# Optimization experiments

Measured on AMD Instinct MI355X. Metric: run time of the kernel, lower is better.

Reference implementation:

```python
import jax, jax.numpy as jnp
import numpy as np

BATCH, NODES, CH_IN, CH_OUT, N_EXPERTS = 8, 8192, 128, 128, 64

def setup_inputs() -> dict:
    key = jax.random.key(0)
    kx, kw, ks = jax.random.split(key, 3)
    x = jax.random.normal(kx, (BATCH, NODES, CH_IN), dtype=jnp.float32)
    # std = fan_in**-0.5 per self_init
    W = jax.random.normal(kw, (N_EXPERTS, CH_OUT, CH_IN), dtype=jnp.float32) * (CH_IN ** -0.5)
    sel = jax.random.randint(ks, (NODES,), 0, N_EXPERTS, dtype=jnp.int64)
    return {"x": x, "sel": sel, "W": W}

def reference(x, sel, W):
    # x: (b, n, j), W[sel]: (n, i, j) -> out: (b, n, i)
    Wsel = W[sel]  # gather a (ch_out, ch_in) matrix per node
    return jnp.einsum('bnj,nij->bni', x, Wsel)
```

## Files before the change

kernel.cpp:

```cpp
#include <hip/hip_runtime.h>

#define BATCH   8
#define NODES   8192
#define CH      128
#define NEXP    64
#define TN      16
#define MAXP    (NODES + NEXP * TN)
#define NTILES  (MAXP / TN)
#define NSORT   64
#define SLICE   (NODES / NSORT)

typedef __attribute__((ext_vector_type(8))) short bf16x8;
typedef __attribute__((ext_vector_type(4))) float f32x4;

typedef const __attribute__((address_space(1))) unsigned int gu32;
typedef __attribute__((address_space(3))) unsigned int lu32;

__device__ __forceinline__ bf16x8 cvt8(f32x4 lo, f32x4 hi) {
    bf16x8 r;
    #pragma unroll
    for (int i = 0; i < 4; ++i) {
        r[i]     = (short)__builtin_bit_cast(unsigned short, static_cast<__bf16>(lo[i]));
        r[i + 4] = (short)__builtin_bit_cast(unsigned short, static_cast<__bf16>(hi[i]));
    }
    return r;
}

__global__ __launch_bounds__(256)
void prep1_kernel(const int* __restrict__ sel, const float* __restrict__ W,
                  short* __restrict__ Wbf, int* __restrict__ sorted,
                  int* __restrict__ gcnt)
{
    const int t   = threadIdx.x;
    const int blk = blockIdx.x;

    #pragma unroll
    for (int i = 0; i < 2; ++i) {
        const int g8  = blk * 512 + i * 256 + t;
        const int e   = g8 >> 11;
        const int row = (g8 & 2047) >> 4;
        const int chk = g8 & 15;
        const float* ws = W + (size_t)g8 * 8;
        f32x4 lo = *reinterpret_cast<const f32x4*>(ws);
        f32x4 hi = *reinterpret_cast<const f32x4*>(ws + 4);
        short* wd = Wbf + ((size_t)e << 14) + row * CH + ((chk ^ (row & 7)) << 3);
        *reinterpret_cast<bf16x8*>(wd) = cvt8(lo, hi);
    }

    {
        const int si = blk * 256 + t;
        if (si < MAXP) sorted[si] = -1;
    }

    if (blk < NSORT) {
        __shared__ int hist[NEXP];
        if (t < NEXP) hist[t] = 0;
        __syncthreads();
        if (t < SLICE) atomicAdd(&hist[sel[blk * SLICE + t]], 1);
        __syncthreads();
        if (t < NEXP) gcnt[blk * NEXP + t] = hist[t];
    }
}

__global__ __launch_bounds__(256)
void prep2_kernel(const int* __restrict__ sel, const int* __restrict__ gcnt,
                  int* __restrict__ sorted)
{
    const int t   = threadIdx.x;
    const int blk = blockIdx.x;

    __shared__ int cursor[NEXP];

    if (t < NEXP) {
        int cnt = 0, own = 0;
        for (int s = 0; s < NSORT; ++s) {
            int g = gcnt[s * NEXP + t];
            own += (s < blk) ? g : 0;
            cnt += g;
        }
        int p = (cnt + TN - 1) & ~(TN - 1);
        int scan = p;
        #pragma unroll
        for (int d = 1; d < NEXP; d <<= 1) {
            int v = __shfl_up(scan, d);
            if (t >= d) scan += v;
        }
        cursor[t] = (scan - p) + own;
    }
    __syncthreads();

    if (t < SLICE) {
        int n = blk * SLICE + t;
        int e = sel[n];
        int pos = atomicAdd(&cursor[e], 1);
        sorted[pos] = n;
    }
}

__global__ __launch_bounds__(256)
void gemm_kernel(const float* __restrict__ x, const int* __restrict__ sel,
                 const short* __restrict__ Wbf, float* __restrict__ out,
                 const int* __restrict__ sorted)
{
    __shared__ short s_w[CH * CH];
    __shared__ int s_nodes[TN];
    __shared__ int s_expert;

    const int tid  = threadIdx.x;
    const int tile = blockIdx.x;

    if (tid < TN) s_nodes[tid] = sorted[tile * TN + tid];
    if (tid == 0) {
        int n0 = sorted[tile * TN];
        s_expert = (n0 >= 0) ? sel[n0] : -1;
    }
    __syncthreads();

    const int e = s_expert;
    if (e < 0) return;

    const int wave = tid >> 6;
    const int lane = tid & 63;
    const int m16  = lane & 15;
    const int quad = lane >> 4;

    int          nodej[2];
    const float* xrow[2];
    #pragma unroll
    for (int jt = 0; jt < 2; ++jt) {
        int j    = wave * 32 + jt * 16 + m16;
        int node = s_nodes[j >> 3];
        int b    = j & 7;
        nodej[jt] = node;
        int nd   = (node >= 0) ? node : 0;
        xrow[jt] = x + ((size_t)(b * NODES + nd)) * CH;
    }

    f32x4 xl[2][4][2];
    #pragma unroll
    for (int jt = 0; jt < 2; ++jt)
        #pragma unroll
        for (int kk = 0; kk < 4; ++kk) {
            const float* p = xrow[jt] + kk * 32 + quad * 8;
            xl[jt][kk][0] = *reinterpret_cast<const f32x4*>(p);
            xl[jt][kk][1] = *reinterpret_cast<const f32x4*>(p + 4);
        }

    {
        const char* gsrc = (const char*)(Wbf + ((size_t)e << 14))
                         + wave * 8192 + lane * 16;
        char* ldst = (char*)s_w + wave * 8192;
        #pragma unroll
        for (int i = 0; i < 8; ++i) {
            __builtin_amdgcn_global_load_lds(
                (gu32*)(gsrc + i * 1024),
                (lu32*)(ldst + i * 1024),
                16, 0, 0);
        }
    }
    __syncthreads();

    bf16x8 xfrag[2][4];
    #pragma unroll
    for (int jt = 0; jt < 2; ++jt)
        #pragma unroll
        for (int kk = 0; kk < 4; ++kk)
            xfrag[jt][kk] = cvt8(xl[jt][kk][0], xl[jt][kk][1]);

    f32x4 acc[2][8];
    #pragma unroll
    for (int jt = 0; jt < 2; ++jt)
        #pragma unroll
        for (int ct = 0; ct < 8; ++ct)
            acc[jt][ct] = (f32x4){0.f, 0.f, 0.f, 0.f};

    #pragma unroll
    for (int kk = 0; kk < 4; ++kk) {
        #pragma unroll
        for (int ct = 0; ct < 8; ++ct) {
            const int row = ct * 16 + m16;
            const bf16x8 wfrag = *reinterpret_cast<const bf16x8*>(
                s_w + row * CH + (((kk * 4 + quad) ^ (row & 7)) << 3));
            acc[0][ct] = __builtin_amdgcn_mfma_f32_16x16x32_bf16(
                             wfrag, xfrag[0][kk], acc[0][ct], 0, 0, 0);
            acc[1][ct] = __builtin_amdgcn_mfma_f32_16x16x32_bf16(
                             wfrag, xfrag[1][kk], acc[1][ct], 0, 0, 0);
        }
    }

    #pragma unroll
    for (int jt = 0; jt < 2; ++jt) {
        int node = nodej[jt];
        if (node < 0) continue;
        int j = wave * 32 + jt * 16 + m16;
        int b = j & 7;
        float* orow = out + ((size_t)(b * NODES + node)) * CH;
        #pragma unroll
        for (int ct = 0; ct < 8; ++ct)
            *reinterpret_cast<f32x4*>(orow + ct * 16 + quad * 4) = acc[jt][ct];
    }
}

extern "C" void kernel_launch(void* const* d_in, const int* in_sizes, int n_in,
                              void* d_out, int out_size, void* d_ws, size_t ws_size,
                              hipStream_t stream)
{
    const float* x   = (const float*)d_in[0];
    const int*   sel = (const int*)  d_in[1];
    const float* W   = (const float*)d_in[2];
    float*       out = (float*)d_out;

    short* Wbf    = (short*)d_ws;
    int*   sorted = (int*)((char*)d_ws + (size_t)NEXP * CH * CH * sizeof(short));
    int*   gcnt   = sorted + MAXP;

    prep1_kernel<<<256, 256, 0, stream>>>(sel, W, Wbf, sorted, gcnt);
    prep2_kernel<<<NSORT, 256, 0, stream>>>(sel, gcnt, sorted);
    gemm_kernel<<<NTILES, 256, 0, stream>>>(x, sel, Wbf, out, sorted);
}
```

Before: 102.2 us.

## Precompute per-tile expert id and drop dependent-load prologue in gemm kernel

The sort pass now writes each tile's expert id into a small array, so the GEMM block reads its expert directly instead of going through sorted→sel. This removes one barrier and a chain of dependent global loads at kernel start. The W tile's async LDS loads are also issued before the x loads, and x loads and output stores use nontemporal hints. prep2 runs with 128 threads and fully unrolls its count loop. The tile-expert array adds a small workspace write during prep.

New measurement: 108.7 us. 1.06x slower.

```diff
diff --git a/kernel.cpp b/kernel.cpp
--- a/kernel.cpp
+++ b/kernel.cpp
@@ -29,7 +29,7 @@
 __global__ __launch_bounds__(256)
 void prep1_kernel(const int* __restrict__ sel, const float* __restrict__ W,
                   short* __restrict__ Wbf, int* __restrict__ sorted,
-                  int* __restrict__ gcnt)
+                  int* __restrict__ texp, int* __restrict__ gcnt)
 {
     const int t   = threadIdx.x;
     const int blk = blockIdx.x;
@@ -49,7 +49,8 @@
 
     {
         const int si = blk * 256 + t;
-        if (si < MAXP) sorted[si] = -1;
+        if (si < MAXP)   sorted[si] = -1;
+        if (si < NTILES) texp[si]   = -1;
     }
 
     if (blk < NSORT) {
@@ -62,9 +63,9 @@
     }
 }
 
-__global__ __launch_bounds__(256)
+__global__ __launch_bounds__(128)
 void prep2_kernel(const int* __restrict__ sel, const int* __restrict__ gcnt,
-                  int* __restrict__ sorted)
+                  int* __restrict__ sorted, int* __restrict__ texp)
 {
     const int t   = threadIdx.x;
     const int blk = blockIdx.x;
@@ -73,6 +74,7 @@
 
     if (t < NEXP) {
         int cnt = 0, own = 0;
+        #pragma unroll
         for (int s = 0; s < NSORT; ++s) {
             int g = gcnt[s * NEXP + t];
             own += (s < blk) ? g : 0;
@@ -94,57 +96,28 @@
         int e = sel[n];
         int pos = atomicAdd(&cursor[e], 1);
         sorted[pos] = n;
+        if ((pos & (TN - 1)) == 0) texp[pos >> 4] = e;
     }
 }
 
 __global__ __launch_bounds__(256)
-void gemm_kernel(const float* __restrict__ x, const int* __restrict__ sel,
-                 const short* __restrict__ Wbf, float* __restrict__ out,
-                 const int* __restrict__ sorted)
+void gemm_kernel(const float* __restrict__ x, const short* __restrict__ Wbf,
+                 float* __restrict__ out, const int* __restrict__ sorted,
+                 const int* __restrict__ texp)
 {
     __shared__ short s_w[CH * CH];
-    __shared__ int s_nodes[TN];
-    __shared__ int s_expert;
 
     const int tid  = threadIdx.x;
     const int tile = blockIdx.x;
 
-    if (tid < TN) s_nodes[tid] = sorted[tile * TN + tid];
-    if (tid == 0) {
-        int n0 = sorted[tile * TN];
-        s_expert = (n0 >= 0) ? sel[n0] : -1;
-    }
-    __syncthreads();
-
-    const int e = s_expert;
+    int e = texp[tile];
     if (e < 0) return;
+    e = __builtin_amdgcn_readfirstlane(e);
 
     const int wave = tid >> 6;
     const int lane = tid & 63;
     const int m16  = lane & 15;
     const int quad = lane >> 4;
-
-    int          nodej[2];
-    const float* xrow[2];
-    #pragma unroll
-    for (int jt = 0; jt < 2; ++jt) {
-        int j    = wave * 32 + jt * 16 + m16;
-        int node = s_nodes[j >> 3];
-        int b    = j & 7;
-        nodej[jt] = node;
-        int nd   = (node >= 0) ? node : 0;
-        xrow[jt] = x + ((size_t)(b * NODES + nd)) * CH;
-    }
-
-    f32x4 xl[2][4][2];
-    #pragma unroll
-    for (int jt = 0; jt < 2; ++jt)
-        #pragma unroll
-        for (int kk = 0; kk < 4; ++kk) {
-            const float* p = xrow[jt] + kk * 32 + quad * 8;
-            xl[jt][kk][0] = *reinterpret_cast<const f32x4*>(p);
-            xl[jt][kk][1] = *reinterpret_cast<const f32x4*>(p + 4);
-        }
 
     {
         const char* gsrc = (const char*)(Wbf + ((size_t)e << 14))
@@ -158,6 +131,31 @@
                 16, 0, 0);
         }
     }
+
+    int          nodej[2];
+    const float* xrow[2];
+    #pragma unroll
+    for (int jt = 0; jt < 2; ++jt) {
+        int j    = wave * 32 + jt * 16 + m16;
+        int node = sorted[tile * TN + (j >> 3)];
+        int b    = j & 7;
+        nodej[jt] = node;
+        int nd   = (node >= 0) ? node : 0;
+        xrow[jt] = x + ((size_t)(b * NODES + nd)) * CH;
+    }
+
+    f32x4 xl[2][4][2];
+    #pragma unroll
+    for (int jt = 0; jt < 2; ++jt)
+        #pragma unroll
+        for (int kk = 0; kk < 4; ++kk) {
+            const float* p = xrow[jt] + kk * 32 + quad * 8;
+            xl[jt][kk][0] = __builtin_nontemporal_load(
+                                reinterpret_cast<const f32x4*>(p));
+            xl[jt][kk][1] = __builtin_nontemporal_load(
+                                reinterpret_cast<const f32x4*>(p) + 1);
+        }
+
     __syncthreads();
 
     bf16x8 xfrag[2][4];
@@ -197,7 +195,8 @@
         float* orow = out + ((size_t)(b * NODES + node)) * CH;
         #pragma unroll
         for (int ct = 0; ct < 8; ++ct)
-            *reinterpret_cast<f32x4*>(orow + ct * 16 + quad * 4) = acc[jt][ct];
+            __builtin_nontemporal_store(acc[jt][ct],
+                reinterpret_cast<f32x4*>(orow + ct * 16 + quad * 4));
     }
 }
 
@@ -213,8 +212,9 @@
     short* Wbf    = (short*)d_ws;
     int*   sorted = (int*)((char*)d_ws + (size_t)NEXP * CH * CH * sizeof(short));
     int*   gcnt   = sorted + MAXP;
-
-    prep1_kernel<<<256, 256, 0, stream>>>(sel, W, Wbf, sorted, gcnt);
-    prep2_kernel<<<NSORT, 256, 0, stream>>>(sel, gcnt, sorted);
-    gemm_kernel<<<NTILES, 256, 0, stream>>>(x, sel, Wbf, out, sorted);
-}
+    int*   texp   = gcnt + NSORT * NEXP;
+
+    prep1_kernel<<<256, 256, 0, stream>>>(sel, W, Wbf, sorted, texp, gcnt);
+    prep2_kernel<<<NSORT, 128, 0, stream>>>(sel, gcnt, sorted, texp);
+    gemm_kernel<<<NTILES, 256, 0, stream>>>(x, Wbf, out, sorted, texp);
+}
```
